# Performance work log

Measured on AMD Instinct MI355X. Metric: run time of the kernel, lower is better.

The kernel has to match this reference:

```python
import jax, jax.numpy as jnp
import numpy as np

LP, LQ, B, D0, H = 128, 128, 64, 150, 150
D = 2 * D0  # in_size after self-concatenation


def setup_inputs() -> dict:
    key = jax.random.key(0)
    ks = jax.random.split(key, 12)
    s = 0.08  # weight scale to keep tanh/sigmoid out of hard saturation
    return {
        "Up": jax.random.normal(ks[0], (LP, B, D0), jnp.float32),
        "Uq": jax.random.normal(ks[1], (LQ, B, D0), jnp.float32),
        "Wp": jax.random.normal(ks[2], (H, D), jnp.float32) * s,
        "Wq": jax.random.normal(ks[3], (H, D), jnp.float32) * s,
        "Wv": jax.random.normal(ks[4], (H, H), jnp.float32) * s,
        "Wg": jax.random.normal(ks[5], (2 * D, 2 * D), jnp.float32) * s,
        "V": jax.random.normal(ks[6], (B, H), jnp.float32) * s,
        "v0": jax.random.normal(ks[7], (B, H), jnp.float32) * s,
        "W_ih": jax.random.normal(ks[8], (3 * H, 2 * D), jnp.float32) * s,
        "W_hh": jax.random.normal(ks[9], (3 * H, H), jnp.float32) * s,
        "b_ih": jax.random.normal(ks[10], (3 * H,), jnp.float32) * s,
        "b_hh": jax.random.normal(ks[11], (3 * H,), jnp.float32) * s,
    }


def reference(Up, Uq, Wp, Wq, Wv, Wg, V, v0, W_ih, W_hh, b_ih, b_hh):
    # self-concat of features, as in the original forward
    Upc = jnp.concatenate([Up, Up], axis=2)  # (LP, B, D)
    Uqc = jnp.concatenate([Uq, Uq], axis=2)  # (LQ, B, D)
    # Wq @ Uq is loop-invariant in the original; hoist it (same math)
    Wuq = jnp.einsum('lbd,hd->lbh', Uqc, Wq)  # (LQ, B, H)

    def step(v, up_i):
        # up_i: (B, D); v: (B, H)
        wup = up_i @ Wp.T                                   # (B, H)
        x = jnp.tanh(wup[None] + Wuq + (v @ Wv.T)[None])    # (LQ, B, H)
        s = jnp.einsum('lbh,bh->bl', x, V)                  # (B, LQ)
        a = jax.nn.softmax(s, axis=1)
        c = jnp.einsum('bl,lbd->bd', a, Uqc)                # (B, D)
        r = jnp.concatenate([up_i, c], axis=1)              # (B, 2D)
        r = jax.nn.sigmoid(r @ Wg.T) * r                    # gated input
        # PyTorch GRUCell math
        gi = r @ W_ih.T + b_ih                              # (B, 3H)
        gh = v @ W_hh.T + b_hh                              # (B, 3H)
        i_r, i_z, i_n = jnp.split(gi, 3, axis=1)
        h_r, h_z, h_n = jnp.split(gh, 3, axis=1)
        rr = jax.nn.sigmoid(i_r + h_r)
        zz = jax.nn.sigmoid(i_z + h_z)
        n = jnp.tanh(i_n + rr * h_n)
        h = (1.0 - zz) * n + zz * v
        return h, h

    _, vs = jax.lax.scan(step, v0, Upc)  # vs: (LP, B, H)
    return vs  # dropout in eval mode = identity
```

## Files before the change

### kernel.cpp

```cpp
#include <hip/hip_runtime.h>
#include <hip/hip_fp16.h>

typedef _Float16 h2_t __attribute__((ext_vector_type(2)));

#define BAR_LGKM() \
  asm volatile("s_waitcnt lgkmcnt(0)\n\ts_barrier" ::: "memory")

__device__ __forceinline__ float dot2f(int w, int x, float acc) {
#if __has_builtin(__builtin_amdgcn_fdot2)
  return __builtin_amdgcn_fdot2(__builtin_bit_cast(h2_t, w),
                                __builtin_bit_cast(h2_t, x), acc, false);
#else
  h2_t a = __builtin_bit_cast(h2_t, w);
  h2_t b = __builtin_bit_cast(h2_t, x);
  return acc + (float)a[0] * (float)b[0] + (float)a[1] * (float)b[1];
#endif
}

__device__ __forceinline__ float rcp_f(float x) {
#if __has_builtin(__builtin_amdgcn_rcpf)
  return __builtin_amdgcn_rcpf(x);
#else
  return 1.0f / x;
#endif
}

__device__ __forceinline__ float fast_tanh(float x) {
  float e = exp2f(x * 2.885390082f);
  return 1.0f - 2.0f * rcp_f(e + 1.0f);
}
__device__ __forceinline__ float fast_sigmoid(float x) {
  return rcp_f(1.0f + exp2f(x * -1.442695041f));
}
__device__ __forceinline__ int packh2(float a, float b) {
  h2_t h;
  h[0] = (_Float16)a;
  h[1] = (_Float16)b;
  return __builtin_bit_cast(int, h);
}

__device__ __forceinline__ int ldi_coh(const int* p) {
  return __hip_atomic_load((int*)p, __ATOMIC_RELAXED, __HIP_MEMORY_SCOPE_AGENT);
}
__device__ __forceinline__ float ldf_coh(const float* p) {
  return __hip_atomic_load((float*)p, __ATOMIC_RELAXED,
                           __HIP_MEMORY_SCOPE_AGENT);
}
__device__ __forceinline__ void sti_coh(int* p, int v) {
  __hip_atomic_store(p, v, __ATOMIC_RELAXED, __HIP_MEMORY_SCOPE_AGENT);
}
__device__ __forceinline__ void stf_coh(float* p, float v) {
  __hip_atomic_store(p, v, __ATOMIC_RELAXED, __HIP_MEMORY_SCOPE_AGENT);
}

#define DOTC(W, X, A)                                                          \
  {                                                                            \
    int4 _x = (X);                                                             \
    A = dot2f((W).x, _x.x, A);                                                 \
    A = dot2f((W).y, _x.y, A);                                                 \
    A = dot2f((W).z, _x.z, A);                                                 \
    A = dot2f((W).w, _x.w, A);                                                 \
  }

__global__ void prep_weights(const float* __restrict__ Wp,
                             const float* __restrict__ Wv,
                             const float* __restrict__ Wg,
                             const float* __restrict__ Wih,
                             const float* __restrict__ Whh,
                             __half* __restrict__ oMa, __half* __restrict__ oWg,
                             __half* __restrict__ oWih,
                             __half* __restrict__ oWhh, int* __restrict__ flags,
                             int* __restrict__ payload) {
  if (blockIdx.x == 0) {
    for (int j = threadIdx.x; j < 1024; j += 256) flags[j] = 0;
  }
  int idx = blockIdx.x * 256 + threadIdx.x;
  const int NMa = 150 * 304, NWg = 600 * 304, NWih = 900 * 304,
            NWhh = 452 * 152;
  if (idx < NMa) {
    int r = idx / 304, c = idx % 304;
    float v = 0.f;
    if (c < 150)
      v = Wp[r * 300 + c] + Wp[r * 300 + 150 + c];
    else if (c >= 152 && c < 302)
      v = Wv[r * 150 + (c - 152)];
    oMa[(c >> 3) * 1200 + r * 8 + (c & 7)] = __float2half(v);
    return;
  }
  idx -= NMa;
  if (idx < NWg) {
    int r = idx / 304, c = idx % 304;
    float v = 0.f;
    if (c < 150)
      v = Wg[r * 600 + c] + Wg[r * 600 + 150 + c];
    else if (c >= 152 && c < 302) {
      int d = c - 152;
      v = Wg[r * 600 + 300 + d] + Wg[r * 600 + 450 + d];
    }
    oWg[(c >> 3) * 4800 + r * 8 + (c & 7)] = __float2half(v);
    return;
  }
  idx -= NWg;
  if (idx < NWih) {
    int s = idx / 304, c = idx % 304;
    int r = s >> 1, off = (s & 1) * 300;
    float v = (c < 300) ? Wih[r * 600 + off + c] : 0.f;
    oWih[(c >> 3) * 7200 + s * 8 + (c & 7)] = __float2half(v);
    return;
  }
  idx -= NWih;
  if (idx < NWhh) {
    int r = idx / 152, c = idx % 152;
    float v = (r < 450 && c < 150) ? Whh[r * 150 + c] : 0.f;
    oWhh[(c >> 3) * 3616 + r * 8 + (c & 7)] = __float2half(v);
  }
}

__global__ __launch_bounds__(256) void prep_wuq(const float* __restrict__ Uq,
                                                const float* __restrict__ Wq,
                                                __half* __restrict__ oWuq,
                                                __half* __restrict__ oUqh) {
  __shared__ float sUql[64 * 150];
  const int l = blockIdx.x, tid = threadIdx.x;
  for (int idx = tid; idx < 9600; idx += 256) sUql[idx] = Uq[l * 9600 + idx];
  __syncthreads();
  for (int idx = tid; idx < 64 * 152; idx += 256) {
    int bb = idx / 152, d = idx % 152;
    float v = (d < 150) ? sUql[bb * 150 + d] : 0.f;
    oUqh[(size_t)bb * 19456 + l * 152 + d] = __float2half(v);
  }
  if (tid < 152) {
    const int h = tid;
    if (h < 150) {
      float wq[150];
#pragma unroll
      for (int d = 0; d < 150; ++d)
        wq[d] = Wq[h * 300 + d] + Wq[h * 300 + 150 + d];
      for (int bb = 0; bb < 64; ++bb) {
        float acc = 0.f;
#pragma unroll
        for (int d = 0; d < 150; ++d) acc += wq[d] * sUql[bb * 150 + d];
        oWuq[(size_t)bb * 19456 + l * 152 + h] = __float2half(acc);
      }
    } else {
      for (int bb = 0; bb < 64; ++bb)
        oWuq[(size_t)bb * 19456 + l * 152 + h] = __float2half(0.f);
    }
  }
}

__device__ __forceinline__ void post_and_wait(int* f4, int q, int target) {
  __syncthreads();
  if (threadIdx.x == 0) sti_coh(&f4[q], target);
  if (threadIdx.x < 4) {
    int spins = 0;
    while (ldi_coh(&f4[threadIdx.x]) < target && ++spins < (1 << 20)) {
      __builtin_amdgcn_s_sleep(1);
    }
  }
  BAR_LGKM();
}

__global__ __launch_bounds__(1024, 1) void pq_main(
    const float* __restrict__ Up, const float* __restrict__ V,
    const float* __restrict__ v0, const float* __restrict__ b_ih,
    const float* __restrict__ b_hh, const int* __restrict__ gWuq,
    const __half* __restrict__ gUqh, const int* __restrict__ gMa,
    const int* __restrict__ gWg, const int* __restrict__ gWih,
    const int* __restrict__ gWhh, int* __restrict__ flags,
    int* __restrict__ payload, float* __restrict__ out) {
  __shared__ __align__(16) float sTV[304];
  __shared__ __align__(16) float sV[152];
  __shared__ __align__(16) float sGh[456];
  __shared__ __align__(16) float sS[128];
  __shared__ __align__(16) float sSS[4];
  __shared__ __align__(16) float sC0[152];
  __shared__ __align__(16) float sU[152];
  __shared__ __align__(16) float sv_[152];
  __shared__ __align__(16) int sXd[152];
  __shared__ __align__(16) int svh[76];
  __shared__ __align__(16) int sRgh[304];
  __shared__ __align__(16) float sGi[456];
  __shared__ __align__(16) float sBih[456];
  __shared__ __align__(16) float sBhh[456];
  extern __shared__ __align__(16) int dynlds[];
  int* sWuq = dynlds;
  __half* sUqh = (__half*)(dynlds + 9728);

  const int t = threadIdx.x;
  const int c = blockIdx.x & 63;
  const int q = blockIdx.x >> 6;
  const int b = c;

  int* myflags = flags + c * 16;
  int* pl = payload + c * 4096;
  float* plS = (float*)pl;
  float* plGh = (float*)(pl + 512);
  float* plGi = (float*)(pl + 1024);

  const int4* MaT4 = (const int4*)gMa;
  const int4* WgT4 = (const int4*)gWg;
  const int4* WihT4 = (const int4*)gWih;
  const int4* WhhT4 = (const int4*)gWhh;

  const int baseR = 113 * q - (q == 3 ? 1 : 0);
  const int cntR = (q < 2) ? 113 : 112;
  const int c_lo = (q == 0) ? 0 : (q == 1) ? 18 : (q == 2) ? 38 : 56;
  const int c_hi = (q == 0) ? 18 : (q == 1) ? 37 : (q == 2) ? 56 : 75;

  int4 a0, a1, a2, a3, a4, a5, a6, a7, a8, a9;
  int4 b0, b1, b2, b3, b4, b5, b6, b7, b8, b9;
  {
    const int4* p;
    int nr, sub, step, nch, row;
    if (t < 152) {
      p = MaT4; nr = 150; step = 4; nch = 38;
      sub = t & 3; row = 38 * q + (t >> 2);
      if (row > 149) row = 149;
    } else if (t < 378) {
      p = WhhT4; nr = 452; step = 2; nch = 19;
      int u2 = t - 152; sub = u2 & 1; row = baseR + (u2 >> 1);
    } else if (t >= 384 && t < 984) {
      p = WgT4; nr = 600; step = 4; nch = 38;
      int u2 = t - 384; sub = u2 & 3; row = 150 * q + (u2 >> 2);
    } else {
      p = MaT4; nr = 150; step = 4; nch = 38; sub = 0; row = 0;
    }
#define LDA(i)                                                                 \
  {                                                                            \
    int cc = sub + step * (i);                                                 \
    if (cc > nch - 1) cc = nch - 1;                                            \
    a##i = p[cc * nr + row];                                                   \
  }
    LDA(0) LDA(1) LDA(2) LDA(3) LDA(4) LDA(5) LDA(6) LDA(7) LDA(8) LDA(9)
#undef LDA
  }
  {
    int row = (t < 900) ? (t >> 1) : 0;
    int sub = (t < 900) ? (t & 1) : 0;
#define LDB(i)                                                                 \
  {                                                                            \
    int cq = c_lo + sub + 2 * (i);                                             \
    if (cq > c_hi) cq = c_hi;                                                  \
    int hf = (cq >= 38) ? 1 : 0;                                               \
    int cc = cq - 38 * hf;                                                     \
    b##i = WihT4[cc * 900 + 2 * row + hf];                                     \
  }
    LDB(0) LDB(1) LDB(2) LDB(3) LDB(4) LDB(5) LDB(6) LDB(7) LDB(8) LDB(9)
#undef LDB
  }

  for (int idx = t; idx < 9728; idx += 1024) sWuq[idx] = gWuq[b * 9728 + idx];
  {
    const int* gU2 = (const int*)(gUqh + (size_t)b * 19456);
    int* sU2 = (int*)sUqh;
    for (int idx = t; idx < 9728; idx += 1024) {
      int lq = idx / 2432, rem = idx - lq * 2432;
      sU2[lq * 2436 + rem] = gU2[idx];
    }
  }
  if (t < 150) {
    sV[t] = V[b * 150 + t];
    float v_ = v0[b * 150 + t];
    sv_[t] = v_;
    float vn = __shfl_down(v_, 1);
    if (!(t & 1)) svh[t >> 1] = packh2(v_, vn);
    float u_ = Up[b * 150 + t];
    sU[t] = u_;
    float un = __shfl_down(u_, 1);
    if (!(t & 1)) sXd[t >> 1] = packh2(u_, un);
  }
  for (int idx = t; idx < 450; idx += 1024) {
    sBih[idx] = b_ih[idx];
    sBhh[idx] = b_hh[idx];
  }
  if (t < 304) {
    sRgh[t] = 0;
    sTV[t] = 0.f;
  }
  if (t == 0) {
    svh[75] = 0;
    sXd[75] = 0;
    sXd[151] = 0;
    sV[150] = 0.f;
    sV[151] = 0.f;
  }
  const int4* sXd4 = (const int4*)sXd;
  const int4* svh4 = (const int4*)svh;
  const int4* sRgh4 = (const int4*)sRgh;
  __syncthreads();

#pragma unroll 1
  for (int i = 0; i < 128; ++i) {
    float unext = 0.f;
    if (t >= 640 && t < 790) {
      int ii = (i < 127) ? (i + 1) : 127;
      unext = Up[ii * 9600 + b * 150 + (t - 640)];
    }

    if (t < 152) {
      int rl = t >> 2, sub = t & 3;
      float acc0 = 0.f, acc1 = 0.f;
#define MAD(i2, A)                                                             \
  {                                                                            \
    int cc = sub + 4 * (i2);                                                   \
    if (cc < 38) {                                                             \
      int4 x = (cc < 19) ? sXd4[cc] : svh4[cc - 19];                           \
      DOTC(a##i2, x, A)                                                        \
    }                                                                          \
  }
      MAD(0, acc0) MAD(1, acc1) MAD(2, acc0) MAD(3, acc1) MAD(4, acc0)
      MAD(5, acc1) MAD(6, acc0) MAD(7, acc1) MAD(8, acc0) MAD(9, acc1)
#undef MAD
      float acc = acc0 + acc1;
      acc += __shfl_xor(acc, 1);
      acc += __shfl_xor(acc, 2);
      float accN = __shfl_down(acc, 4);
      if (sub == 0 && !(rl & 1)) {
        int w = 19 * q + (rl >> 1);
        int h = 38 * q + rl;
        float4 tv;
        tv.x = acc;
        tv.y = accN;
        tv.z = sV[h];
        tv.w = sV[h + 1];
        ((float4*)sTV)[w] = tv;
      }
    } else if (t < 378) {
      int u2 = t - 152;
      int rl = u2 >> 1, sub = u2 & 1;
      int r = baseR + rl;
      float acc0 = 0.f, acc1 = 0.f;
#define HHD(i2, A)                                                             \
  {                                                                            \
    int cc = sub + 2 * (i2);                                                   \
    if (cc < 19) DOTC(a##i2, svh4[cc], A)                                      \
  }
      HHD(0, acc0) HHD(1, acc1) HHD(2, acc0) HHD(3, acc1) HHD(4, acc0)
      HHD(5, acc1) HHD(6, acc0) HHD(7, acc1) HHD(8, acc0) HHD(9, acc1)
#undef HHD
      float acc = acc0 + acc1;
      acc += __shfl_xor(acc, 1);
      if (sub == 0 && rl < cntR) stf_coh(&plGh[r], acc + sBhh[r]);
    }
    BAR_LGKM();

    {
      const int l = t >> 3, sub = t & 7;
      const int base = l * 76;
      float acc = 0.f;
#pragma unroll
      for (int k = 0; k < 3; ++k) {
        int wl = sub + 8 * k;
        if (wl < 19) {
          int w = 19 * q + wl;
          int qq = sWuq[base + w];
          float4 tv = ((const float4*)sTV)[w];
          h2_t hq = __builtin_bit_cast(h2_t, qq);
          float x0 = (float)hq[0] + tv.x;
          float x1 = (float)hq[1] + tv.y;
          acc += fast_tanh(x0) * tv.z;
          acc += fast_tanh(x1) * tv.w;
        }
      }
      acc += __shfl_xor(acc, 1);
      acc += __shfl_xor(acc, 2);
      acc += __shfl_xor(acc, 4);
      if (sub == 0) stf_coh(&plS[128 * q + l], acc);
    }
    post_and_wait(myflags, q, i + 1);
    if (t < 128) {
      float s = ldf_coh(&plS[t]) + ldf_coh(&plS[128 + t]) +
                ldf_coh(&plS[256 + t]) + ldf_coh(&plS[384 + t]);
      float e = exp2f(s * 1.442695041f);
      sS[t] = e;
      float es = e;
#pragma unroll
      for (int o = 1; o < 64; o <<= 1) es += __shfl_xor(es, o);
      if (t == 0) sSS[0] = es;
      if (t == 64) sSS[1] = es;
    } else if (t >= 128 && t < 578) {
      sGh[t - 128] = ldf_coh(&plGh[t - 128]);
    }
    BAR_LGKM();

    if (t < 600) {
      const int d = t >> 2, lq = t & 3;
      const __half* src = sUqh + lq * 4872 + d;
      const float* a = sS + lq * 32;
      float acc = 0.f;
#pragma unroll
      for (int j = 0; j < 32; ++j) {
        acc += a[j] * __half2float(src[j * 152]);
      }
      acc += __shfl_xor(acc, 1);
      acc += __shfl_xor(acc, 2);
      float inv = rcp_f(sSS[0] + sSS[1]);
      float c0 = acc * inv;
      float cn = __shfl_down(c0, 4);
      if (lq == 0) {
        sC0[d] = c0;
        if (!(d & 1)) sXd[76 + (d >> 1)] = packh2(c0, cn);
      }
    }
    BAR_LGKM();

    if (t >= 384 && t < 984) {
      int u2 = t - 384;
      int rl = u2 >> 2, sub = u2 & 3;
      int j = 150 * q + rl;
      float acc0 = 0.f, acc1 = 0.f;
#define WGD(i2, A)                                                             \
  {                                                                            \
    int cc = sub + 4 * (i2);                                                   \
    if (cc < 38) DOTC(a##i2, sXd4[cc], A)                                      \
  }
      WGD(0, acc0) WGD(1, acc1) WGD(2, acc0) WGD(3, acc1) WGD(4, acc0)
      WGD(5, acc1) WGD(6, acc0) WGD(7, acc1) WGD(8, acc0) WGD(9, acc1)
#undef WGD
      float acc = acc0 + acc1;
      acc += __shfl_xor(acc, 1);
      acc += __shfl_xor(acc, 2);
      if (sub == 0) {
        float rb;
        if (j < 150)
          rb = sU[j];
        else if (j < 300)
          rb = sU[j - 150];
        else if (j < 450)
          rb = sC0[j - 300];
        else
          rb = sC0[j - 450];
        float rg = rb * fast_sigmoid(acc);
        ((__half*)sRgh)[(j < 300) ? j : (j + 4)] = __float2half(rg);
      }
    }
    BAR_LGKM();

    if (t < 900) {
      int row = t >> 1, sub = t & 1;
      float acc0 = 0.f, acc1 = 0.f;
#define IHD(i2, A)                                                             \
  {                                                                            \
    int cq = c_lo + sub + 2 * (i2);                                            \
    if (cq <= c_hi) DOTC(b##i2, sRgh4[cq], A)                                  \
  }
      IHD(0, acc0) IHD(1, acc1) IHD(2, acc0) IHD(3, acc1) IHD(4, acc0)
      IHD(5, acc1) IHD(6, acc0) IHD(7, acc1) IHD(8, acc0) IHD(9, acc1)
#undef IHD
      float acc = acc0 + acc1;
      acc += __shfl_xor(acc, 1);
      if (!sub) stf_coh(&plGi[456 * q + row], acc);
    }
    post_and_wait(myflags + 4, q, i + 1);
    if (t < 450) {
      float g0 = ldf_coh(&plGi[t]);
      float g1 = ldf_coh(&plGi[456 + t]);
      float g2 = ldf_coh(&plGi[912 + t]);
      float g3 = ldf_coh(&plGi[1368 + t]);
      sGi[t] = g0 + g1 + g2 + g3 + sBih[t];
    }
    BAR_LGKM();

    if (t < 150) {
      float ir = sGi[t], iz = sGi[150 + t], in_ = sGi[300 + t];
      float hr = sGh[t], hz = sGh[150 + t], hn = sGh[300 + t];
      float rr = fast_sigmoid(ir + hr);
      float zz = fast_sigmoid(iz + hz);
      float nn = fast_tanh(in_ + rr * hn);
      float vold = sv_[t];
      float hv = nn + zz * (vold - nn);
      if (q == 0) out[i * 9600 + b * 150 + t] = hv;
      sv_[t] = hv;
      float hv1 = __shfl_down(hv, 1);
      if (!(t & 1)) svh[t >> 1] = packh2(hv, hv1);
    } else if (t >= 640 && t < 790) {
      int t2 = t - 640;
      sU[t2] = unext;
      float un = __shfl_down(unext, 1);
      if (!(t2 & 1)) sXd[t2 >> 1] = packh2(unext, un);
    }
    BAR_LGKM();
  }
}

extern "C" void kernel_launch(void* const* d_in, const int* in_sizes, int n_in,
                              void* d_out, int out_size, void* d_ws,
                              size_t ws_size, hipStream_t stream) {
  const float* Up = (const float*)d_in[0];
  const float* Uq = (const float*)d_in[1];
  const float* Wp = (const float*)d_in[2];
  const float* Wq = (const float*)d_in[3];
  const float* Wv = (const float*)d_in[4];
  const float* Wg = (const float*)d_in[5];
  const float* V = (const float*)d_in[6];
  const float* v0 = (const float*)d_in[7];
  const float* Wih = (const float*)d_in[8];
  const float* Whh = (const float*)d_in[9];
  const float* bih = (const float*)d_in[10];
  const float* bhh = (const float*)d_in[11];

  char* ws = (char*)d_ws;
  __half* wsWuq = (__half*)(ws);
  __half* wsUqh = (__half*)(ws + 2490368);
  __half* wsMa = (__half*)(ws + 4980736);
  __half* wsWg = (__half*)(ws + 5071936);
  __half* wsWih = (__half*)(ws + 5436736);
  __half* wsWhh = (__half*)(ws + 5983936);
  int* wsFlags = (int*)(ws + 6121472);
  int* wsPayload = (int*)(ws + 6125568);

  (void)hipFuncSetAttribute((const void*)pq_main,
                            hipFuncAttributeMaxDynamicSharedMemorySize, 77888);

  prep_weights<<<2228, 256, 0, stream>>>(Wp, Wv, Wg, Wih, Whh, wsMa, wsWg,
                                         wsWih, wsWhh, wsFlags, wsPayload);
  prep_wuq<<<128, 256, 0, stream>>>(Uq, Wq, wsWuq, wsUqh);
  pq_main<<<256, 1024, 77888, stream>>>(Up, V, v0, bih, bhh, (const int*)wsWuq,
                                        wsUqh, (const int*)wsMa,
                                        (const int*)wsWg, (const int*)wsWih,
                                        (const int*)wsWhh, wsFlags, wsPayload,
                                        (float*)d_out);
}
```

Measured before the change: 1.291 ms.

## Replicate attention scoring per block to drop one cross-block barrier per step

Each of the four cooperating blocks per batch row now computes the full 150-wide Wp/Wv projection and all attention scores locally, keeping the Ma weights in LDS. This removes the first inter-block flag handshake and the payload exchange of partial scores in every timestep. Gh and Gi payloads are double-buffered by step parity so the single remaining barrier is enough, and the spin loop no longer sleeps. The Uq half-precision context values are now read from global memory instead of LDS so Ma fits. In exchange each block does four times the attention tanh and projection work, uses more LDS, and adds global-memory latency to the context reduction.

```diff
diff --git a/kernel.cpp b/kernel.cpp
--- a/kernel.cpp
+++ b/kernel.cpp
@@ -149,18 +149,6 @@
   }
 }
 
-__device__ __forceinline__ void post_and_wait(int* f4, int q, int target) {
-  __syncthreads();
-  if (threadIdx.x == 0) sti_coh(&f4[q], target);
-  if (threadIdx.x < 4) {
-    int spins = 0;
-    while (ldi_coh(&f4[threadIdx.x]) < target && ++spins < (1 << 20)) {
-      __builtin_amdgcn_s_sleep(1);
-    }
-  }
-  BAR_LGKM();
-}
-
 __global__ __launch_bounds__(1024, 1) void pq_main(
     const float* __restrict__ Up, const float* __restrict__ V,
     const float* __restrict__ v0, const float* __restrict__ b_ih,
@@ -169,7 +157,7 @@
     const int* __restrict__ gWg, const int* __restrict__ gWih,
     const int* __restrict__ gWhh, int* __restrict__ flags,
     int* __restrict__ payload, float* __restrict__ out) {
-  __shared__ __align__(16) float sTV[304];
+  __shared__ __align__(16) float sTpre[152];
   __shared__ __align__(16) float sV[152];
   __shared__ __align__(16) float sGh[456];
   __shared__ __align__(16) float sS[128];
@@ -184,8 +172,8 @@
   __shared__ __align__(16) float sBih[456];
   __shared__ __align__(16) float sBhh[456];
   extern __shared__ __align__(16) int dynlds[];
-  int* sWuq = dynlds;
-  __half* sUqh = (__half*)(dynlds + 9728);
+  int4* lMa4 = (int4*)dynlds;
+  int* sWuq = dynlds + 22800;
 
   const int t = threadIdx.x;
   const int c = blockIdx.x & 63;
@@ -193,10 +181,11 @@
   const int b = c;
 
   int* myflags = flags + c * 16;
-  int* pl = payload + c * 4096;
-  float* plS = (float*)pl;
-  float* plGh = (float*)(pl + 512);
-  float* plGi = (float*)(pl + 1024);
+  int* pl = payload + c * 6144;
+  float* plGh0 = (float*)pl;
+  float* plGh1 = (float*)(pl + 512);
+  float* plGi0 = (float*)(pl + 1024);
+  float* plGi1 = (float*)(pl + 2848);
 
   const int4* MaT4 = (const int4*)gMa;
   const int4* WgT4 = (const int4*)gWg;
@@ -213,18 +202,14 @@
   {
     const int4* p;
     int nr, sub, step, nch, row;
-    if (t < 152) {
-      p = MaT4; nr = 150; step = 4; nch = 38;
-      sub = t & 3; row = 38 * q + (t >> 2);
-      if (row > 149) row = 149;
-    } else if (t < 378) {
+    if (t >= 158 && t < 384) {
       p = WhhT4; nr = 452; step = 2; nch = 19;
-      int u2 = t - 152; sub = u2 & 1; row = baseR + (u2 >> 1);
+      int u2 = t - 158; sub = u2 & 1; row = baseR + (u2 >> 1);
     } else if (t >= 384 && t < 984) {
       p = WgT4; nr = 600; step = 4; nch = 38;
       int u2 = t - 384; sub = u2 & 3; row = 150 * q + (u2 >> 2);
     } else {
-      p = MaT4; nr = 150; step = 4; nch = 38; sub = 0; row = 0;
+      p = WhhT4; nr = 452; step = 2; nch = 19; sub = 0; row = 0;
     }
 #define LDA(i)                                                                 \
   {                                                                            \
@@ -250,15 +235,8 @@
 #undef LDB
   }
 
+  for (int idx = t; idx < 5700; idx += 1024) lMa4[idx] = MaT4[idx];
   for (int idx = t; idx < 9728; idx += 1024) sWuq[idx] = gWuq[b * 9728 + idx];
-  {
-    const int* gU2 = (const int*)(gUqh + (size_t)b * 19456);
-    int* sU2 = (int*)sUqh;
-    for (int idx = t; idx < 9728; idx += 1024) {
-      int lq = idx / 2432, rem = idx - lq * 2432;
-      sU2[lq * 2436 + rem] = gU2[idx];
-    }
-  }
   if (t < 150) {
     sV[t] = V[b * 150 + t];
     float v_ = v0[b * 150 + t];
@@ -274,10 +252,8 @@
     sBih[idx] = b_ih[idx];
     sBhh[idx] = b_hh[idx];
   }
-  if (t < 304) {
-    sRgh[t] = 0;
-    sTV[t] = 0.f;
-  }
+  if (t < 304) sRgh[t] = 0;
+  if (t < 152) sTpre[t] = 0.f;
   if (t == 0) {
     svh[75] = 0;
     sXd[75] = 0;
@@ -292,42 +268,28 @@
 
 #pragma unroll 1
   for (int i = 0; i < 128; ++i) {
+    float* plGhP = (i & 1) ? plGh1 : plGh0;
+    float* plGiP = (i & 1) ? plGi1 : plGi0;
     float unext = 0.f;
     if (t >= 640 && t < 790) {
       int ii = (i < 127) ? (i + 1) : 127;
       unext = Up[ii * 9600 + b * 150 + (t - 640)];
     }
 
-    if (t < 152) {
-      int rl = t >> 2, sub = t & 3;
+    if (t < 150) {
       float acc0 = 0.f, acc1 = 0.f;
-#define MAD(i2, A)                                                             \
-  {                                                                            \
-    int cc = sub + 4 * (i2);                                                   \
-    if (cc < 38) {                                                             \
-      int4 x = (cc < 19) ? sXd4[cc] : svh4[cc - 19];                           \
-      DOTC(a##i2, x, A)                                                        \
-    }                                                                          \
-  }
-      MAD(0, acc0) MAD(1, acc1) MAD(2, acc0) MAD(3, acc1) MAD(4, acc0)
-      MAD(5, acc1) MAD(6, acc0) MAD(7, acc1) MAD(8, acc0) MAD(9, acc1)
-#undef MAD
-      float acc = acc0 + acc1;
-      acc += __shfl_xor(acc, 1);
-      acc += __shfl_xor(acc, 2);
-      float accN = __shfl_down(acc, 4);
-      if (sub == 0 && !(rl & 1)) {
-        int w = 19 * q + (rl >> 1);
-        int h = 38 * q + rl;
-        float4 tv;
-        tv.x = acc;
-        tv.y = accN;
-        tv.z = sV[h];
-        tv.w = sV[h + 1];
-        ((float4*)sTV)[w] = tv;
-      }
-    } else if (t < 378) {
-      int u2 = t - 152;
+#pragma unroll
+      for (int cc = 0; cc < 38; cc += 2) {
+        int4 w0 = lMa4[cc * 150 + t];
+        int4 w1 = lMa4[(cc + 1) * 150 + t];
+        int4 x0 = (cc < 19) ? sXd4[cc] : svh4[cc - 19];
+        int4 x1 = (cc + 1 < 19) ? sXd4[cc + 1] : svh4[cc + 1 - 19];
+        DOTC(w0, x0, acc0)
+        DOTC(w1, x1, acc1)
+      }
+      sTpre[t] = acc0 + acc1;
+    } else if (t < 384 && t >= 158) {
+      int u2 = t - 158;
       int rl = u2 >> 1, sub = u2 & 1;
       int r = baseR + rl;
       float acc0 = 0.f, acc1 = 0.f;
@@ -341,7 +303,7 @@
 #undef HHD
       float acc = acc0 + acc1;
       acc += __shfl_xor(acc, 1);
-      if (sub == 0 && rl < cntR) stf_coh(&plGh[r], acc + sBhh[r]);
+      if (sub == 0 && rl < cntR) stf_coh(&plGhP[r], acc + sBhh[r]);
     }
     BAR_LGKM();
 
@@ -350,43 +312,38 @@
       const int base = l * 76;
       float acc = 0.f;
 #pragma unroll
-      for (int k = 0; k < 3; ++k) {
-        int wl = sub + 8 * k;
-        if (wl < 19) {
-          int w = 19 * q + wl;
+      for (int k = 0; k < 10; ++k) {
+        int w = sub + 8 * k;
+        if (w < 76) {
           int qq = sWuq[base + w];
-          float4 tv = ((const float4*)sTV)[w];
+          float2 tp = ((const float2*)sTpre)[w];
+          float2 vv = ((const float2*)sV)[w];
           h2_t hq = __builtin_bit_cast(h2_t, qq);
-          float x0 = (float)hq[0] + tv.x;
-          float x1 = (float)hq[1] + tv.y;
-          acc += fast_tanh(x0) * tv.z;
-          acc += fast_tanh(x1) * tv.w;
+          acc += fast_tanh((float)hq[0] + tp.x) * vv.x;
+          acc += fast_tanh((float)hq[1] + tp.y) * vv.y;
         }
       }
       acc += __shfl_xor(acc, 1);
       acc += __shfl_xor(acc, 2);
       acc += __shfl_xor(acc, 4);
-      if (sub == 0) stf_coh(&plS[128 * q + l], acc);
-    }
-    post_and_wait(myflags, q, i + 1);
+      if (sub == 0) sS[l] = acc;
+    }
+    BAR_LGKM();
+
     if (t < 128) {
-      float s = ldf_coh(&plS[t]) + ldf_coh(&plS[128 + t]) +
-                ldf_coh(&plS[256 + t]) + ldf_coh(&plS[384 + t]);
-      float e = exp2f(s * 1.442695041f);
+      float e = exp2f(sS[t] * 1.442695041f);
       sS[t] = e;
       float es = e;
 #pragma unroll
       for (int o = 1; o < 64; o <<= 1) es += __shfl_xor(es, o);
       if (t == 0) sSS[0] = es;
       if (t == 64) sSS[1] = es;
-    } else if (t >= 128 && t < 578) {
-      sGh[t - 128] = ldf_coh(&plGh[t - 128]);
     }
     BAR_LGKM();
 
     if (t < 600) {
       const int d = t >> 2, lq = t & 3;
-      const __half* src = sUqh + lq * 4872 + d;
+      const __half* src = gUqh + (size_t)b * 19456 + (size_t)(lq * 32) * 152 + d;
       const float* a = sS + lq * 32;
       float acc = 0.f;
 #pragma unroll
@@ -450,15 +407,24 @@
 #undef IHD
       float acc = acc0 + acc1;
       acc += __shfl_xor(acc, 1);
-      if (!sub) stf_coh(&plGi[456 * q + row], acc);
-    }
-    post_and_wait(myflags + 4, q, i + 1);
+      if (!sub) stf_coh(&plGiP[456 * q + row], acc);
+    }
+    __syncthreads();
+    if (t == 0) sti_coh(&myflags[q], i + 1);
+    if (t < 4) {
+      int spins = 0;
+      while (ldi_coh(&myflags[t]) < i + 1 && ++spins < (1 << 20)) {
+      }
+    }
+    BAR_LGKM();
     if (t < 450) {
-      float g0 = ldf_coh(&plGi[t]);
-      float g1 = ldf_coh(&plGi[456 + t]);
-      float g2 = ldf_coh(&plGi[912 + t]);
-      float g3 = ldf_coh(&plGi[1368 + t]);
+      float g0 = ldf_coh(&plGiP[t]);
+      float g1 = ldf_coh(&plGiP[456 + t]);
+      float g2 = ldf_coh(&plGiP[912 + t]);
+      float g3 = ldf_coh(&plGiP[1368 + t]);
       sGi[t] = g0 + g1 + g2 + g3 + sBih[t];
+    } else if (t >= 512 && t < 962) {
+      sGh[t - 512] = ldf_coh(&plGhP[t - 512]);
     }
     BAR_LGKM();
 
@@ -511,14 +477,14 @@
   int* wsPayload = (int*)(ws + 6125568);
 
   (void)hipFuncSetAttribute((const void*)pq_main,
-                            hipFuncAttributeMaxDynamicSharedMemorySize, 77888);
+                            hipFuncAttributeMaxDynamicSharedMemorySize, 130112);
 
   prep_weights<<<2228, 256, 0, stream>>>(Wp, Wv, Wg, Wih, Whh, wsMa, wsWg,
                                          wsWih, wsWhh, wsFlags, wsPayload);
   prep_wuq<<<128, 256, 0, stream>>>(Uq, Wq, wsWuq, wsUqh);
-  pq_main<<<256, 1024, 77888, stream>>>(Up, V, v0, bih, bhh, (const int*)wsWuq,
-                                        wsUqh, (const int*)wsMa,
-                                        (const int*)wsWg, (const int*)wsWih,
-                                        (const int*)wsWhh, wsFlags, wsPayload,
-                                        (float*)d_out);
-}
+  pq_main<<<256, 1024, 130112, stream>>>(Up, V, v0, bih, bhh, (const int*)wsWuq,
+                                         wsUqh, (const int*)wsMa,
+                                         (const int*)wsWg, (const int*)wsWih,
+                                         (const int*)wsWhh, wsFlags, wsPayload,
+                                         (float*)d_out);
+}
```

Result: slower. 2.783 ms (+115.5%).
